# Kernel tuning notes

Measured on AMD Instinct MI355X. Metric: run time of the kernel, lower is better.

The kernel has to match this reference:

```python
import math
import jax, jax.numpy as jnp
import numpy as np

RM = 100.0      # r_max
RN = 1000       # r_dsc
LMAX = 2
MATCH_FRAC = 0.1
PARA1 = 1.0
RD = RM / RN    # radial step
NE = 4096       # batch of trial energies


def setup_inputs() -> dict:
    key = jax.random.key(0)
    # small negative energies (bound-state regime) to keep the exponential
    # Numerov growth over 900 steps within fp32 range
    init_energy = -(jax.random.uniform(key, (NE,), dtype=jnp.float32) * 0.01 + 0.005)
    return {"init_energy": init_energy}


def _disc_solve(sol0, factor, limit):
    # sol0: (5, n_e, L) initial 5-point window; factor: (rn, n_e, L)
    # Numerov-style 4-step recurrence, vectorized coefficients + lax.scan
    c = 3.0 / 40.0 * RD ** 2
    idx = jnp.arange(1, limit - 5)
    f0 = factor[idx]
    f1 = factor[idx + 1]
    f2 = factor[idx + 2]
    f3 = factor[idx + 3]
    f4 = factor[idx + 4]
    denom = 1.0 - c * f4
    a = -1.0 + c * f0 / denom
    b = 2.0 + (13.0 / 15.0) * RD ** 2 * f1 / denom
    cc = -2.0 + (7.0 / 60.0) * RD ** 2 * f2 / denom
    d = 2.0 + (13.0 / 15.0) * RD ** 2 * f3 / denom

    def step(prev, coef):
        ca, cb, ccc, cd = coef
        new4 = ca * prev[1] + cb * prev[2] + ccc * prev[3] + cd * prev[4]
        new = jnp.concatenate([prev[1:], new4[None]], axis=0)  # shift window
        return new, new

    _, rest = jax.lax.scan(step, sol0, (a, b, cc, d))
    return jnp.concatenate([sol0[None], rest], axis=0)  # (limit-5, 5, n_e, L)


def _derivative(func, at):
    return (25.0 * func[at - 1] - 48.0 * func[at - 2] + 36.0 * func[at - 3]
            - 16.0 * func[at - 4] + 3.0 * func[at - 5]) / (12.0 * RD)


def _integrate(func):
    # faithful to original: integrand squares `func` again (func is u**2 here)
    M = func.shape[0] // 4 - 1
    g0 = func[0:4 * M:4]
    g1 = func[1:4 * M:4]
    g2 = func[2:4 * M:4]
    g3 = func[3:4 * M:4]
    g4 = func[4::4][:M]
    integrand = (7.0 * (g0 ** 2 + g4 ** 2) + 32.0 * (g1 ** 2 + g3 ** 2)
                 + 12.0 * g2) * (2.0 * RD / 45.0)
    return integrand.sum(axis=0)


def _forward(init_energy):
    L = LMAX + 1
    dt = init_energy.dtype
    n_e = init_energy.shape[0]
    r = jnp.linspace(RM / RN, RM, RN, dtype=dt).reshape(RN, 1, 1)
    l = jnp.arange(L, dtype=dt).reshape(1, 1, L)

    energy = jnp.broadcast_to(init_energy[:, None], (n_e, L))  # (n_e, L)
    e_val = energy[None]                                       # (1, n_e, L)
    # coulomb potential -1/r; factor: (rn, n_e, L)
    factor = l * (l + 1) / r ** 2 + PARA1 * (-e_val - 1.0 / r)

    # left (r->0) initial window: u ~ r^(l+1) + r^(l+2)/(2(l+1)) * (-para_1)
    r0 = jnp.linspace(RD, 5 * RD, 5, dtype=dt).reshape(5, 1, 1)
    u_zero_init = jnp.broadcast_to(
        r0 ** (l + 1) - r0 ** (l + 2) / (2.0 * (l + 1)) * PARA1, (5, n_e, L))

    # right (r->r_max) initial window: r * truncated spherical-bessel series
    r_inf = jnp.linspace(RM - 4 * RD, RM, 5, dtype=dt).reshape(5, 1, 1)
    fact = jnp.array([math.prod([2 * li + 1 for li in range(lm + 1)])
                      for lm in range(L)], dtype=dt)  # [1, 3, 15]
    x = r_inf * jnp.sqrt(jnp.abs(e_val))              # (5, n_e, L)
    base = x ** l / fact
    t1 = x ** 2 / 2.0 / (2 * l + 3)
    t2 = (x ** 2 / 2.0) ** 2 / (2.0 * (2 * l + 3) * (2 * l + 5))
    u_infty_init = jnp.broadcast_to(r_inf * (base * (1.0 + t1 + t2)), (5, n_e, L))

    match = int(RN * MATCH_FRAC)  # 100
    uz = _disc_solve(u_zero_init, factor, match)                     # (95, 5, n_e, L)
    ui = _disc_solve(u_infty_init, factor[::-1], RN - match)[::-1]   # (895, 5, n_e, L)
    u_zero = jnp.concatenate([uz[0], uz[:, 4]], axis=0)    # (100, n_e, L)
    u_infty = jnp.concatenate([ui[0], ui[:, 4]], axis=0)   # (900, n_e, L)

    lfunc_in = _derivative(u_zero, match) / u_zero[-1]
    # faithful: the trailing flip acts on the energy axis of the (n_e, L) result
    lfunc_out = _derivative(u_infty[::-1], RN - match)[::-1] / u_infty[0]
    integ_in = _integrate(u_zero ** 2)
    integ_out = _integrate(u_infty ** 2)
    delta = -(lfunc_out - lfunc_in) / (integ_in / u_zero[-1] ** 2
                                       + integ_out / u_infty[0] ** 2)
    return (energy + delta, u_zero, u_infty)


def reference(init_energy):
    return _forward(init_energy)
```

## Files before the change

### kernel.cpp

```cpp
#include <hip/hip_runtime.h>


namespace {
constexpr int kNE    = 4096;
constexpr int kNCH   = kNE * 3;
constexpr int kMatch = 100;
constexpr float kC   = 3.0f / 40.0f * 0.01f;
constexpr float kK1  = 13.0f / 15.0f * 0.01f;
constexpr float kK2  = 7.0f / 60.0f * 0.01f;
constexpr int kSeg        = 32;
constexpr int kCPB        = 16;
constexpr int kZeroBlocks = kNCH / 512;
constexpr int kInfBlocks  = kNCH / kCPB;
}

__device__ __forceinline__ float rcp_f(float x) { return __builtin_amdgcn_rcpf(x); }
__device__ __forceinline__ float rcp_nr(float x) {
    float r = __builtin_amdgcn_rcpf(x);
    return fmaf(fmaf(-x, r, 1.0f), r, r);
}

__global__ __launch_bounds__(512, 4) void solve_kernel(const float* __restrict__ energy,
                                                       float* __restrict__ out,
                                                       float* __restrict__ ws)
{
    __shared__ __align__(16) float gtp[908];
    __shared__ float sM[kSeg][4][kCPB][4];
    float* sF = &sM[0][0][0][0];

    const int bid = (int)blockIdx.x;
    const int tid = (int)threadIdx.x;
    float* uzero = out + kNCH;
    float* uinf  = out + kNCH + (size_t)kMatch * kNCH;

    if (bid < kZeroBlocks) {
        const int t  = bid * 512 + tid;
        const int l  = t % 3;
        const int ei = t / 3;
        const float e = energy[ei], negE = -e;
        const float ll1 = (float)(l * (l + 1));
        const float rdiv = (l == 0) ? 0.5f : ((l == 1) ? 0.25f : (1.0f/6.0f));
        float p0,p1,p2,p3,p4;
        {
            float pw[5];
            #pragma unroll
            for (int k = 0; k < 5; ++k) {
                float r = 0.1f * (float)(k + 1);
                float rl1 = (l == 0) ? r : ((l == 1) ? r*r : r*r*r);
                pw[k] = rl1 - (rl1 * r) * rdiv;
                uzero[(size_t)k * kNCH + t] = pw[k];
            }
            uzero[(size_t)5 * kNCH + t] = pw[4];
            p0=pw[0]; p1=pw[1]; p2=pw[2]; p3=pw[3]; p4=pw[4];
        }
        float acc4, acc2;
        {
            float q0=p0*p0, q1=p1*p1, q2=p2*p2, q3=p3*p3, q4=p4*p4;
            acc4 = 7.0f*q0*q0 + 32.0f*q1*q1 + 32.0f*q3*q3 + 14.0f*q4*q4 + 32.0f*q4*q4;
            acc2 = q2;
        }
        float f0, f1, f2, f3;
        {
            float i1 = rcp_f(0.2f), i2 = rcp_f(0.3f), i3 = rcp_f(0.4f), i4 = rcp_f(0.5f);
            f0 = fmaf(i1, fmaf(ll1, i1, -1.0f), negE);
            f1 = fmaf(i2, fmaf(ll1, i2, -1.0f), negE);
            f2 = fmaf(i3, fmaf(ll1, i3, -1.0f), negE);
            f3 = fmaf(i4, fmaf(ll1, i4, -1.0f), negE);
        }
        float* ptr = uzero + (size_t)6 * kNCH + t;
        #pragma unroll 4
        for (int j = 5; j <= 98; ++j) {
            float ri = rcp_f(fmaf((float)j, 0.1f, 0.1f));
            float f4 = fmaf(ri, fmaf(ll1, ri, -1.0f), negE);
            float iv = rcp_f(fmaf(-kC, f4, 1.0f));
            float a  = fmaf(kC  * f0, iv, -1.0f);
            float b  = fmaf(kK1 * f1, iv,  2.0f);
            float cc = fmaf(kK2 * f2, iv, -2.0f);
            float d  = fmaf(kK1 * f3, iv,  2.0f);
            float nw = fmaf(d, p4, fmaf(cc, p3, fmaf(b, p2, a * p1)));
            *ptr = nw; ptr += kNCH;
            float v2 = nw*nw, v4 = v2*v2;
            if (j <= 94) {
                int m = (j + 1) & 3;
                if (m == 2)      acc2 += v2;
                else if (m == 0) acc4 += 14.0f * v4;
                else             acc4 += 32.0f * v4;
            } else if (j == 95) {
                acc4 += 7.0f * v4;
            }
            f0 = f1; f1 = f2; f2 = f3; f3 = f4;
            p0 = p1; p1 = p2; p2 = p3; p3 = p4; p4 = nw;
        }
        float integ = fmaf(12.0f, acc2, acc4) * (2.0f * 0.1f / 45.0f);
        float deriv = fmaf(25.0f, p4, fmaf(-48.0f, p3, fmaf(36.0f, p2,
                      fmaf(-16.0f, p1, 3.0f * p0)))) * (1.0f / 1.2f);
        ws[2 * kNCH + t] = deriv / p4;
        ws[3 * kNCH + t] = integ / (p4 * p4);
        return;
    }

    for (int k = tid; k < 908; k += 512) {
        int j = k - 3;
        gtp[k] = (j >= 1 && j <= 898) ? rcp_nr(fmaf((float)j, -0.1f, 100.0f)) : 1.0f;
    }
    __syncthreads();

    const int b = bid - kZeroBlocks;
    const int g = tid & (kCPB - 1);
    const int s = tid >> 4;
    const int t = b * kCPB + g;
    const int l  = t % 3;
    const int ei = t / 3;
    const float e = energy[ei], negE = -e;
    const float ll1 = (float)(l * (l + 1));
    const int jstart = 5 + 28 * s;

    const float4* gq = (const float4*)(&gtp[jstart + 3]);
    float ff0, ff1, ff2, ff3;
    {
        const float4 wF = *(const float4*)(&gtp[jstart - 1]);
        ff0 = fmaf(wF.x, fmaf(ll1, wF.x, -1.0f), negE);
        ff1 = fmaf(wF.y, fmaf(ll1, wF.y, -1.0f), negE);
        ff2 = fmaf(wF.z, fmaf(ll1, wF.z, -1.0f), negE);
        ff3 = fmaf(wF.w, fmaf(ll1, wF.w, -1.0f), negE);
    }
    float F0 = ff0, F1 = ff1, F2 = ff2, F3 = ff3;

    float ca, cb, cc_, cd;
#define COEF(RI, FA,FB,FC,FD) \
    { float f4 = fmaf(RI, fmaf(ll1, RI, -1.0f), negE); \
      float x  = kC * f4; \
      float iv = fmaf(x, x, x) + 1.0f; \
      ca  = fmaf(kC  * FA, iv, -1.0f); \
      cb  = fmaf(kK1 * FB, iv,  2.0f); \
      cc_ = fmaf(kK2 * FC, iv, -2.0f); \
      cd  = fmaf(kK1 * FD, iv,  2.0f); \
      FA = f4; }

#define MSTEP(RI, FA,FB,FC,FD, RA,RB,RC,RD) \
    { COEF(RI, FA,FB,FC,FD) \
      RA[0] = fmaf(cd,RD[0], fmaf(cc_,RC[0], fmaf(cb,RB[0], ca*RA[0]))); \
      RA[1] = fmaf(cd,RD[1], fmaf(cc_,RC[1], fmaf(cb,RB[1], ca*RA[1]))); \
      RA[2] = fmaf(cd,RD[2], fmaf(cc_,RC[2], fmaf(cb,RB[2], ca*RA[2]))); \
      RA[3] = fmaf(cd,RD[3], fmaf(cc_,RC[3], fmaf(cb,RB[3], ca*RA[3]))); }

    if (s != 31) {
        float ra[4] = {1,0,0,0}, rb[4] = {0,1,0,0}, rc[4] = {0,0,1,0}, rd[4] = {0,0,0,1};
        #pragma unroll
        for (int gi = 0; gi < 7; ++gi) {
            const float4 w = gq[gi];
            MSTEP(w.x, F0,F1,F2,F3, ra,rb,rc,rd)
            MSTEP(w.y, F1,F2,F3,F0, rb,rc,rd,ra)
            MSTEP(w.z, F2,F3,F0,F1, rc,rd,ra,rb)
            MSTEP(w.w, F3,F0,F1,F2, rd,ra,rb,rc)
        }
        *(float4*)&sM[s][0][g][0] = make_float4(ra[0], ra[1], ra[2], ra[3]);
        *(float4*)&sM[s][1][g][0] = make_float4(rb[0], rb[1], rb[2], rb[3]);
        *(float4*)&sM[s][2][g][0] = make_float4(rc[0], rc[1], rc[2], rc[3]);
        *(float4*)&sM[s][3][g][0] = make_float4(rd[0], rd[1], rd[2], rd[3]);
    }
    __syncthreads();

    if (s == 0) {
        const float se  = sqrtf(fabsf(e));
        const float rfc = (l == 0) ? 1.0f : ((l == 1) ? (1.0f/3.0f) : (1.0f/15.0f));
        const float rt1 = (l == 0) ? (1.0f/3.0f) : ((l == 1) ? (1.0f/5.0f) : (1.0f/7.0f));
        const float rt2 = (l == 0) ? (1.0f/30.0f) : ((l == 1) ? (1.0f/70.0f) : (1.0f/126.0f));
        float pw[5];
        #pragma unroll
        for (int k = 0; k < 5; ++k) {
            float rinf = 99.6f + 0.1f * (float)k;
            float x  = rinf * se;
            float xl = (l == 0) ? 1.0f : ((l == 1) ? x : x * x);
            float h  = x * x * 0.5f;
            pw[k] = rinf * (xl * rfc * (1.0f + h * rt1 + (h * h) * rt2));
        }
        uinf[(size_t)899 * kNCH + t] = pw[4];
        float st0 = pw[1], st1 = pw[2], st2 = pw[3], st3 = pw[4];
        for (int ss = 0; ss < kSeg; ++ss) {
            if (ss < kSeg - 1) {
                float4 M0 = *(const float4*)&sM[ss][0][g][0];
                float4 M1 = *(const float4*)&sM[ss][1][g][0];
                float4 M2 = *(const float4*)&sM[ss][2][g][0];
                float4 M3 = *(const float4*)&sM[ss][3][g][0];
                *(float4*)&sM[ss][0][g][0] = make_float4(st0, st1, st2, st3);
                float n0 = fmaf(M0.w,st3, fmaf(M0.z,st2, fmaf(M0.y,st1, M0.x*st0)));
                float n1 = fmaf(M1.w,st3, fmaf(M1.z,st2, fmaf(M1.y,st1, M1.x*st0)));
                float n2 = fmaf(M2.w,st3, fmaf(M2.z,st2, fmaf(M2.y,st1, M2.x*st0)));
                float n3 = fmaf(M3.w,st3, fmaf(M3.z,st2, fmaf(M3.y,st1, M3.x*st0)));
                st0 = n0; st1 = n1; st2 = n2; st3 = n3;
            } else {
                *(float4*)&sM[ss][0][g][0] = make_float4(st0, st1, st2, st3);
            }
        }
    }
    __syncthreads();

    float W0[4] = {0.0f, 32.0f, 14.0f, 32.0f};
    float V0[4] = {1.0f, 0.0f, 0.0f, 0.0f};
    float WR[4] = {0.0f, 32.0f, 14.0f, 32.0f};
    float VR[4] = {1.0f, 0.0f, 0.0f, 0.0f};
    if (s == 0) {
        W0[0]=0.0f; V0[0]=0.0f; W0[1]=0.0f; W0[2]=7.0f; W0[3]=32.0f;
    }

    F0 = ff0; F1 = ff1; F2 = ff2; F3 = ff3;
    float p0, p1, p2, p3;
    {
        float4 P = *(const float4*)&sM[s][0][g][0];
        p0 = P.x; p1 = P.y; p2 = P.z; p3 = P.w;
    }
    float acc4 = 0.0f, acc2 = 0.0f;
    float* ptr = uinf + (size_t)(903 - jstart) * kNCH + t;
#define RSTEPW(RI, FA,FB,FC,FD, PA,PB,PC,PD, W,V,K) \
    { COEF(RI, FA,FB,FC,FD) \
      float nw = fmaf(cd,PD, fmaf(cc_,PC, fmaf(cb,PB, ca*PA))); \
      PA = nw; *ptr = nw; ptr -= kNCH; \
      float v2 = nw*nw, v4 = v2*v2; \
      acc4 = fmaf(W[K], v4, acc4); \
      acc2 = fmaf(V[K], v2, acc2); }
#define PG(G, W, V) \
    { const float4 w = gq[G]; \
      RSTEPW(w.x, F0,F1,F2,F3, p0,p1,p2,p3, W,V,0) \
      RSTEPW(w.y, F1,F2,F3,F0, p1,p2,p3,p0, W,V,1) \
      RSTEPW(w.z, F2,F3,F0,F1, p2,p3,p0,p1, W,V,2) \
      RSTEPW(w.w, F3,F0,F1,F2, p3,p0,p1,p2, W,V,3) }

    PG(0, W0, V0)
    PG(1, WR, VR) PG(2, WR, VR) PG(3, WR, VR) PG(4, WR, VR) PG(5, WR, VR)
    float h0 = p1, h1 = p2, h2 = p3;
    if (s == 31) { WR[2] = 0.0f; WR[3] = 0.0f; }
    PG(6, WR, VR)
    float h3 = p0, h4 = p1;
#undef PG
#undef RSTEPW

    {
        float2 rr; rr.x = acc4; rr.y = acc2;
        *(float2*)&sF[s * 256 + 64 + 4 * g] = rr;
    }
    __syncthreads();

    if (s == kSeg - 1) {
        float a4 = 0.0f, a2 = 0.0f;
        #pragma unroll
        for (int ss = 0; ss < kSeg; ++ss) {
            float2 rr = *(const float2*)&sF[ss * 256 + 64 + 4 * g];
            a4 += rr.x; a2 += rr.y;
        }
        uinf[(size_t)0 * kNCH + t] = h0;
        uinf[(size_t)1 * kNCH + t] = h1;
        uinf[(size_t)2 * kNCH + t] = h2;
        uinf[(size_t)3 * kNCH + t] = h3;
        uinf[(size_t)4 * kNCH + t] = h4;
        float q0 = h0*h0, q1 = h1*h1, q2 = h2*h2, q3 = h3*h3, q4 = h4*h4;
        a4 += 7.0f*q0*q0 + 32.0f*q1*q1 + 32.0f*q3*q3 + 14.0f*q4*q4;
        a2 += q2;
        float integ = fmaf(12.0f, a2, a4) * (2.0f * 0.1f / 45.0f);
        float deriv = fmaf(25.0f, h0, fmaf(-48.0f, h1, fmaf(36.0f, h2,
                      fmaf(-16.0f, h3, 3.0f * h4)))) * (1.0f / 1.2f);
        ws[t]        = deriv / h0;
        ws[kNCH + t] = integ / (h0 * h0);
    }
#undef MSTEP
#undef COEF
}

__global__ __launch_bounds__(256) void final_kernel(const float* __restrict__ energy,
                                                    const float* __restrict__ ws,
                                                    float* __restrict__ out)
{
    int t = (int)blockIdx.x * 256 + (int)threadIdx.x;
    if (t >= kNCH) return;
    int l = t % 3, ei = t / 3;
    float lf_out = ws[(kNE - 1 - ei) * 3 + l];
    float lf_in  = ws[2 * kNCH + t];
    float den    = ws[kNCH + t] + ws[3 * kNCH + t];
    out[t] = energy[ei] - (lf_out - lf_in) / den;
}

extern "C" void kernel_launch(void* const* d_in, const int* in_sizes, int n_in,
                              void* d_out, int out_size, void* d_ws, size_t ws_size,
                              hipStream_t stream) {
    (void)in_sizes; (void)n_in; (void)out_size; (void)ws_size;
    const float* energy = (const float*)d_in[0];
    float* out = (float*)d_out;
    float* ws  = (float*)d_ws;
    solve_kernel<<<kZeroBlocks + kInfBlocks, 512, 0, stream>>>(energy, out, ws);
    final_kernel<<<kNCH / 256, 256, 0, stream>>>(energy, ws, out);
}
```

Measured before the change: 85.82 us.

## Process two channels per thread in the u_infty segmented solve

Each thread in the outward (u_infty) blocks now handles two adjacent channels instead of one, which halves the number of inf blocks. The per-step recurrence and the transfer-matrix products for the two channels are interleaved to expose more ILP, and u_infty stores become float2 writes so global memory traffic is wider. This costs roughly double the register use and extra shared memory per block, which may lower occupancy.

```diff
diff --git a/kernel.cpp b/kernel.cpp
--- a/kernel.cpp
+++ b/kernel.cpp
@@ -9,9 +9,9 @@
 constexpr float kK1  = 13.0f / 15.0f * 0.01f;
 constexpr float kK2  = 7.0f / 60.0f * 0.01f;
 constexpr int kSeg        = 32;
-constexpr int kCPB        = 16;
+constexpr int kPPB        = 16;
 constexpr int kZeroBlocks = kNCH / 512;
-constexpr int kInfBlocks  = kNCH / kCPB;
+constexpr int kInfBlocks  = kNCH / (2 * kPPB);
 }
 
 __device__ __forceinline__ float rcp_f(float x) { return __builtin_amdgcn_rcpf(x); }
@@ -25,8 +25,9 @@
                                                        float* __restrict__ ws)
 {
     __shared__ __align__(16) float gtp[908];
-    __shared__ float sM[kSeg][4][kCPB][4];
-    float* sF = &sM[0][0][0][0];
+    __shared__ float sMA[kSeg][4][kPPB][4];
+    __shared__ float sMB[kSeg][4][kPPB][4];
+    __shared__ float4 sRed[kSeg][kPPB];
 
     const int bid = (int)blockIdx.x;
     const int tid = (int)threadIdx.x;
@@ -105,92 +106,130 @@
     }
     __syncthreads();
 
-    const int b = bid - kZeroBlocks;
-    const int g = tid & (kCPB - 1);
-    const int s = tid >> 4;
-    const int t = b * kCPB + g;
-    const int l  = t % 3;
-    const int ei = t / 3;
-    const float e = energy[ei], negE = -e;
-    const float ll1 = (float)(l * (l + 1));
+    const int b  = bid - kZeroBlocks;
+    const int g  = tid & (kPPB - 1);
+    const int s  = tid >> 4;
+    const int t2 = b * (2 * kPPB) + g * 2;
+    const int lA = t2 % 3,  lB = (t2 + 1) % 3;
+    const float eA = energy[t2 / 3], eB = energy[(t2 + 1) / 3];
+    const float negEA = -eA, negEB = -eB;
+    const float ll1A = (float)(lA * (lA + 1));
+    const float ll1B = (float)(lB * (lB + 1));
     const int jstart = 5 + 28 * s;
 
     const float4* gq = (const float4*)(&gtp[jstart + 3]);
-    float ff0, ff1, ff2, ff3;
+    float fA0, fA1, fA2, fA3, fB0, fB1, fB2, fB3;
     {
         const float4 wF = *(const float4*)(&gtp[jstart - 1]);
-        ff0 = fmaf(wF.x, fmaf(ll1, wF.x, -1.0f), negE);
-        ff1 = fmaf(wF.y, fmaf(ll1, wF.y, -1.0f), negE);
-        ff2 = fmaf(wF.z, fmaf(ll1, wF.z, -1.0f), negE);
-        ff3 = fmaf(wF.w, fmaf(ll1, wF.w, -1.0f), negE);
-    }
-    float F0 = ff0, F1 = ff1, F2 = ff2, F3 = ff3;
-
-    float ca, cb, cc_, cd;
-#define COEF(RI, FA,FB,FC,FD) \
-    { float f4 = fmaf(RI, fmaf(ll1, RI, -1.0f), negE); \
-      float x  = kC * f4; \
-      float iv = fmaf(x, x, x) + 1.0f; \
-      ca  = fmaf(kC  * FA, iv, -1.0f); \
-      cb  = fmaf(kK1 * FB, iv,  2.0f); \
-      cc_ = fmaf(kK2 * FC, iv, -2.0f); \
-      cd  = fmaf(kK1 * FD, iv,  2.0f); \
-      FA = f4; }
-
-#define MSTEP(RI, FA,FB,FC,FD, RA,RB,RC,RD) \
-    { COEF(RI, FA,FB,FC,FD) \
-      RA[0] = fmaf(cd,RD[0], fmaf(cc_,RC[0], fmaf(cb,RB[0], ca*RA[0]))); \
-      RA[1] = fmaf(cd,RD[1], fmaf(cc_,RC[1], fmaf(cb,RB[1], ca*RA[1]))); \
-      RA[2] = fmaf(cd,RD[2], fmaf(cc_,RC[2], fmaf(cb,RB[2], ca*RA[2]))); \
-      RA[3] = fmaf(cd,RD[3], fmaf(cc_,RC[3], fmaf(cb,RB[3], ca*RA[3]))); }
+        fA0 = fmaf(wF.x, fmaf(ll1A, wF.x, -1.0f), negEA);
+        fA1 = fmaf(wF.y, fmaf(ll1A, wF.y, -1.0f), negEA);
+        fA2 = fmaf(wF.z, fmaf(ll1A, wF.z, -1.0f), negEA);
+        fA3 = fmaf(wF.w, fmaf(ll1A, wF.w, -1.0f), negEA);
+        fB0 = fmaf(wF.x, fmaf(ll1B, wF.x, -1.0f), negEB);
+        fB1 = fmaf(wF.y, fmaf(ll1B, wF.y, -1.0f), negEB);
+        fB2 = fmaf(wF.z, fmaf(ll1B, wF.z, -1.0f), negEB);
+        fB3 = fmaf(wF.w, fmaf(ll1B, wF.w, -1.0f), negEB);
+    }
+    float FA0 = fA0, FA1 = fA1, FA2 = fA2, FA3 = fA3;
+    float FB0 = fB0, FB1 = fB1, FB2 = fB2, FB3 = fB3;
+
+    float caA, cbA, ccA, cdA, caB, cbB, ccB, cdB;
+#define COEF2(RI, A0,A1,A2,A3, B0,B1,B2,B3) \
+    { float f4A = fmaf(RI, fmaf(ll1A, RI, -1.0f), negEA); \
+      float f4B = fmaf(RI, fmaf(ll1B, RI, -1.0f), negEB); \
+      float xA = kC * f4A, xB = kC * f4B; \
+      float ivA = fmaf(xA, xA, xA) + 1.0f; \
+      float ivB = fmaf(xB, xB, xB) + 1.0f; \
+      caA = fmaf(kC  * A0, ivA, -1.0f);  caB = fmaf(kC  * B0, ivB, -1.0f); \
+      cbA = fmaf(kK1 * A1, ivA,  2.0f);  cbB = fmaf(kK1 * B1, ivB,  2.0f); \
+      ccA = fmaf(kK2 * A2, ivA, -2.0f);  ccB = fmaf(kK2 * B2, ivB, -2.0f); \
+      cdA = fmaf(kK1 * A3, ivA,  2.0f);  cdB = fmaf(kK1 * B3, ivB,  2.0f); \
+      A0 = f4A; B0 = f4B; }
+
+#define MSTEP2(RI, A0,A1,A2,A3, B0,B1,B2,B3, RA,RB,RC,RD, QA,QB,QC,QD) \
+    { COEF2(RI, A0,A1,A2,A3, B0,B1,B2,B3) \
+      RA[0] = fmaf(cdA,RD[0], fmaf(ccA,RC[0], fmaf(cbA,RB[0], caA*RA[0]))); \
+      QA[0] = fmaf(cdB,QD[0], fmaf(ccB,QC[0], fmaf(cbB,QB[0], caB*QA[0]))); \
+      RA[1] = fmaf(cdA,RD[1], fmaf(ccA,RC[1], fmaf(cbA,RB[1], caA*RA[1]))); \
+      QA[1] = fmaf(cdB,QD[1], fmaf(ccB,QC[1], fmaf(cbB,QB[1], caB*QA[1]))); \
+      RA[2] = fmaf(cdA,RD[2], fmaf(ccA,RC[2], fmaf(cbA,RB[2], caA*RA[2]))); \
+      QA[2] = fmaf(cdB,QD[2], fmaf(ccB,QC[2], fmaf(cbB,QB[2], caB*QA[2]))); \
+      RA[3] = fmaf(cdA,RD[3], fmaf(ccA,RC[3], fmaf(cbA,RB[3], caA*RA[3]))); \
+      QA[3] = fmaf(cdB,QD[3], fmaf(ccB,QC[3], fmaf(cbB,QB[3], caB*QA[3]))); }
 
     if (s != 31) {
-        float ra[4] = {1,0,0,0}, rb[4] = {0,1,0,0}, rc[4] = {0,0,1,0}, rd[4] = {0,0,0,1};
+        float raA[4]={1,0,0,0}, rbA[4]={0,1,0,0}, rcA[4]={0,0,1,0}, rdA[4]={0,0,0,1};
+        float raB[4]={1,0,0,0}, rbB[4]={0,1,0,0}, rcB[4]={0,0,1,0}, rdB[4]={0,0,0,1};
         #pragma unroll
         for (int gi = 0; gi < 7; ++gi) {
             const float4 w = gq[gi];
-            MSTEP(w.x, F0,F1,F2,F3, ra,rb,rc,rd)
-            MSTEP(w.y, F1,F2,F3,F0, rb,rc,rd,ra)
-            MSTEP(w.z, F2,F3,F0,F1, rc,rd,ra,rb)
-            MSTEP(w.w, F3,F0,F1,F2, rd,ra,rb,rc)
-        }
-        *(float4*)&sM[s][0][g][0] = make_float4(ra[0], ra[1], ra[2], ra[3]);
-        *(float4*)&sM[s][1][g][0] = make_float4(rb[0], rb[1], rb[2], rb[3]);
-        *(float4*)&sM[s][2][g][0] = make_float4(rc[0], rc[1], rc[2], rc[3]);
-        *(float4*)&sM[s][3][g][0] = make_float4(rd[0], rd[1], rd[2], rd[3]);
-    }
+            MSTEP2(w.x, FA0,FA1,FA2,FA3, FB0,FB1,FB2,FB3, raA,rbA,rcA,rdA, raB,rbB,rcB,rdB)
+            MSTEP2(w.y, FA1,FA2,FA3,FA0, FB1,FB2,FB3,FB0, rbA,rcA,rdA,raA, rbB,rcB,rdB,raB)
+            MSTEP2(w.z, FA2,FA3,FA0,FA1, FB2,FB3,FB0,FB1, rcA,rdA,raA,rbA, rcB,rdB,raB,rbB)
+            MSTEP2(w.w, FA3,FA0,FA1,FA2, FB3,FB0,FB1,FB2, rdA,raA,rbA,rcA, rdB,raB,rbB,rcB)
+        }
+        *(float4*)&sMA[s][0][g][0] = make_float4(raA[0], raA[1], raA[2], raA[3]);
+        *(float4*)&sMA[s][1][g][0] = make_float4(rbA[0], rbA[1], rbA[2], rbA[3]);
+        *(float4*)&sMA[s][2][g][0] = make_float4(rcA[0], rcA[1], rcA[2], rcA[3]);
+        *(float4*)&sMA[s][3][g][0] = make_float4(rdA[0], rdA[1], rdA[2], rdA[3]);
+        *(float4*)&sMB[s][0][g][0] = make_float4(raB[0], raB[1], raB[2], raB[3]);
+        *(float4*)&sMB[s][1][g][0] = make_float4(rbB[0], rbB[1], rbB[2], rbB[3]);
+        *(float4*)&sMB[s][2][g][0] = make_float4(rcB[0], rcB[1], rcB[2], rcB[3]);
+        *(float4*)&sMB[s][3][g][0] = make_float4(rdB[0], rdB[1], rdB[2], rdB[3]);
+    }
+#undef MSTEP2
     __syncthreads();
 
     if (s == 0) {
-        const float se  = sqrtf(fabsf(e));
-        const float rfc = (l == 0) ? 1.0f : ((l == 1) ? (1.0f/3.0f) : (1.0f/15.0f));
-        const float rt1 = (l == 0) ? (1.0f/3.0f) : ((l == 1) ? (1.0f/5.0f) : (1.0f/7.0f));
-        const float rt2 = (l == 0) ? (1.0f/30.0f) : ((l == 1) ? (1.0f/70.0f) : (1.0f/126.0f));
-        float pw[5];
-        #pragma unroll
-        for (int k = 0; k < 5; ++k) {
-            float rinf = 99.6f + 0.1f * (float)k;
-            float x  = rinf * se;
-            float xl = (l == 0) ? 1.0f : ((l == 1) ? x : x * x);
-            float h  = x * x * 0.5f;
-            pw[k] = rinf * (xl * rfc * (1.0f + h * rt1 + (h * h) * rt2));
-        }
-        uinf[(size_t)899 * kNCH + t] = pw[4];
-        float st0 = pw[1], st1 = pw[2], st2 = pw[3], st3 = pw[4];
+        float stA0, stA1, stA2, stA3, stB0, stB1, stB2, stB3;
+        {
+            const float seA = sqrtf(fabsf(eA)), seB = sqrtf(fabsf(eB));
+            const float rfcA = (lA == 0) ? 1.0f : ((lA == 1) ? (1.0f/3.0f) : (1.0f/15.0f));
+            const float rt1A = (lA == 0) ? (1.0f/3.0f) : ((lA == 1) ? (1.0f/5.0f) : (1.0f/7.0f));
+            const float rt2A = (lA == 0) ? (1.0f/30.0f) : ((lA == 1) ? (1.0f/70.0f) : (1.0f/126.0f));
+            const float rfcB = (lB == 0) ? 1.0f : ((lB == 1) ? (1.0f/3.0f) : (1.0f/15.0f));
+            const float rt1B = (lB == 0) ? (1.0f/3.0f) : ((lB == 1) ? (1.0f/5.0f) : (1.0f/7.0f));
+            const float rt2B = (lB == 0) ? (1.0f/30.0f) : ((lB == 1) ? (1.0f/70.0f) : (1.0f/126.0f));
+            float pwA[5], pwB[5];
+            #pragma unroll
+            for (int k = 0; k < 5; ++k) {
+                float rinf = 99.6f + 0.1f * (float)k;
+                float xA = rinf * seA, xB = rinf * seB;
+                float xlA = (lA == 0) ? 1.0f : ((lA == 1) ? xA : xA * xA);
+                float xlB = (lB == 0) ? 1.0f : ((lB == 1) ? xB : xB * xB);
+                float hA = xA * xA * 0.5f, hB = xB * xB * 0.5f;
+                pwA[k] = rinf * (xlA * rfcA * (1.0f + hA * rt1A + (hA * hA) * rt2A));
+                pwB[k] = rinf * (xlB * rfcB * (1.0f + hB * rt1B + (hB * hB) * rt2B));
+            }
+            *(float2*)&uinf[(size_t)899 * kNCH + t2] = make_float2(pwA[4], pwB[4]);
+            stA0 = pwA[1]; stA1 = pwA[2]; stA2 = pwA[3]; stA3 = pwA[4];
+            stB0 = pwB[1]; stB1 = pwB[2]; stB2 = pwB[3]; stB3 = pwB[4];
+        }
         for (int ss = 0; ss < kSeg; ++ss) {
             if (ss < kSeg - 1) {
-                float4 M0 = *(const float4*)&sM[ss][0][g][0];
-                float4 M1 = *(const float4*)&sM[ss][1][g][0];
-                float4 M2 = *(const float4*)&sM[ss][2][g][0];
-                float4 M3 = *(const float4*)&sM[ss][3][g][0];
-                *(float4*)&sM[ss][0][g][0] = make_float4(st0, st1, st2, st3);
-                float n0 = fmaf(M0.w,st3, fmaf(M0.z,st2, fmaf(M0.y,st1, M0.x*st0)));
-                float n1 = fmaf(M1.w,st3, fmaf(M1.z,st2, fmaf(M1.y,st1, M1.x*st0)));
-                float n2 = fmaf(M2.w,st3, fmaf(M2.z,st2, fmaf(M2.y,st1, M2.x*st0)));
-                float n3 = fmaf(M3.w,st3, fmaf(M3.z,st2, fmaf(M3.y,st1, M3.x*st0)));
-                st0 = n0; st1 = n1; st2 = n2; st3 = n3;
+                float4 MA0 = *(const float4*)&sMA[ss][0][g][0];
+                float4 MA1 = *(const float4*)&sMA[ss][1][g][0];
+                float4 MA2 = *(const float4*)&sMA[ss][2][g][0];
+                float4 MA3 = *(const float4*)&sMA[ss][3][g][0];
+                float4 MB0 = *(const float4*)&sMB[ss][0][g][0];
+                float4 MB1 = *(const float4*)&sMB[ss][1][g][0];
+                float4 MB2 = *(const float4*)&sMB[ss][2][g][0];
+                float4 MB3 = *(const float4*)&sMB[ss][3][g][0];
+                *(float4*)&sMA[ss][0][g][0] = make_float4(stA0, stA1, stA2, stA3);
+                *(float4*)&sMB[ss][0][g][0] = make_float4(stB0, stB1, stB2, stB3);
+                float nA0 = fmaf(MA0.w,stA3, fmaf(MA0.z,stA2, fmaf(MA0.y,stA1, MA0.x*stA0)));
+                float nA1 = fmaf(MA1.w,stA3, fmaf(MA1.z,stA2, fmaf(MA1.y,stA1, MA1.x*stA0)));
+                float nA2 = fmaf(MA2.w,stA3, fmaf(MA2.z,stA2, fmaf(MA2.y,stA1, MA2.x*stA0)));
+                float nA3 = fmaf(MA3.w,stA3, fmaf(MA3.z,stA2, fmaf(MA3.y,stA1, MA3.x*stA0)));
+                float nB0 = fmaf(MB0.w,stB3, fmaf(MB0.z,stB2, fmaf(MB0.y,stB1, MB0.x*stB0)));
+                float nB1 = fmaf(MB1.w,stB3, fmaf(MB1.z,stB2, fmaf(MB1.y,stB1, MB1.x*stB0)));
+                float nB2 = fmaf(MB2.w,stB3, fmaf(MB2.z,stB2, fmaf(MB2.y,stB1, MB2.x*stB0)));
+                float nB3 = fmaf(MB3.w,stB3, fmaf(MB3.z,stB2, fmaf(MB3.y,stB1, MB3.x*stB0)));
+                stA0 = nA0; stA1 = nA1; stA2 = nA2; stA3 = nA3;
+                stB0 = nB0; stB1 = nB1; stB2 = nB2; stB3 = nB3;
             } else {
-                *(float4*)&sM[ss][0][g][0] = make_float4(st0, st1, st2, st3);
+                *(float4*)&sMA[ss][0][g][0] = make_float4(stA0, stA1, stA2, stA3);
+                *(float4*)&sMB[ss][0][g][0] = make_float4(stB0, stB1, stB2, stB3);
             }
         }
     }
@@ -204,66 +243,76 @@
         W0[0]=0.0f; V0[0]=0.0f; W0[1]=0.0f; W0[2]=7.0f; W0[3]=32.0f;
     }
 
-    F0 = ff0; F1 = ff1; F2 = ff2; F3 = ff3;
-    float p0, p1, p2, p3;
+    FA0 = fA0; FA1 = fA1; FA2 = fA2; FA3 = fA3;
+    FB0 = fB0; FB1 = fB1; FB2 = fB2; FB3 = fB3;
+    float pA0, pA1, pA2, pA3, pB0, pB1, pB2, pB3;
     {
-        float4 P = *(const float4*)&sM[s][0][g][0];
-        p0 = P.x; p1 = P.y; p2 = P.z; p3 = P.w;
-    }
-    float acc4 = 0.0f, acc2 = 0.0f;
-    float* ptr = uinf + (size_t)(903 - jstart) * kNCH + t;
-#define RSTEPW(RI, FA,FB,FC,FD, PA,PB,PC,PD, W,V,K) \
-    { COEF(RI, FA,FB,FC,FD) \
-      float nw = fmaf(cd,PD, fmaf(cc_,PC, fmaf(cb,PB, ca*PA))); \
-      PA = nw; *ptr = nw; ptr -= kNCH; \
-      float v2 = nw*nw, v4 = v2*v2; \
-      acc4 = fmaf(W[K], v4, acc4); \
-      acc2 = fmaf(V[K], v2, acc2); }
+        float4 PA = *(const float4*)&sMA[s][0][g][0];
+        float4 PB = *(const float4*)&sMB[s][0][g][0];
+        pA0 = PA.x; pA1 = PA.y; pA2 = PA.z; pA3 = PA.w;
+        pB0 = PB.x; pB1 = PB.y; pB2 = PB.z; pB3 = PB.w;
+    }
+    float acc4A = 0.0f, acc2A = 0.0f, acc4B = 0.0f, acc2B = 0.0f;
+    float* ptr = uinf + (size_t)(903 - jstart) * kNCH + t2;
+#define RSTEP2(RI, A0,A1,A2,A3, B0,B1,B2,B3, PA,PB,PC,PD, QA,QB,QC,QD, W,V,K) \
+    { COEF2(RI, A0,A1,A2,A3, B0,B1,B2,B3) \
+      float nwA = fmaf(cdA,PD, fmaf(ccA,PC, fmaf(cbA,PB, caA*PA))); \
+      float nwB = fmaf(cdB,QD, fmaf(ccB,QC, fmaf(cbB,QB, caB*QA))); \
+      PA = nwA; QA = nwB; \
+      *(float2*)ptr = make_float2(nwA, nwB); ptr -= kNCH; \
+      float v2A = nwA*nwA, v4A = v2A*v2A; \
+      float v2B = nwB*nwB, v4B = v2B*v2B; \
+      acc4A = fmaf(W[K], v4A, acc4A);  acc4B = fmaf(W[K], v4B, acc4B); \
+      acc2A = fmaf(V[K], v2A, acc2A);  acc2B = fmaf(V[K], v2B, acc2B); }
 #define PG(G, W, V) \
     { const float4 w = gq[G]; \
-      RSTEPW(w.x, F0,F1,F2,F3, p0,p1,p2,p3, W,V,0) \
-      RSTEPW(w.y, F1,F2,F3,F0, p1,p2,p3,p0, W,V,1) \
-      RSTEPW(w.z, F2,F3,F0,F1, p2,p3,p0,p1, W,V,2) \
-      RSTEPW(w.w, F3,F0,F1,F2, p3,p0,p1,p2, W,V,3) }
+      RSTEP2(w.x, FA0,FA1,FA2,FA3, FB0,FB1,FB2,FB3, pA0,pA1,pA2,pA3, pB0,pB1,pB2,pB3, W,V,0) \
+      RSTEP2(w.y, FA1,FA2,FA3,FA0, FB1,FB2,FB3,FB0, pA1,pA2,pA3,pA0, pB1,pB2,pB3,pB0, W,V,1) \
+      RSTEP2(w.z, FA2,FA3,FA0,FA1, FB2,FB3,FB0,FB1, pA2,pA3,pA0,pA1, pB2,pB3,pB0,pB1, W,V,2) \
+      RSTEP2(w.w, FA3,FA0,FA1,FA2, FB3,FB0,FB1,FB2, pA3,pA0,pA1,pA2, pB3,pB0,pB1,pB2, W,V,3) }
 
     PG(0, W0, V0)
     PG(1, WR, VR) PG(2, WR, VR) PG(3, WR, VR) PG(4, WR, VR) PG(5, WR, VR)
-    float h0 = p1, h1 = p2, h2 = p3;
+    float hA0 = pA1, hA1 = pA2, hA2 = pA3;
+    float hB0 = pB1, hB1 = pB2, hB2 = pB3;
     if (s == 31) { WR[2] = 0.0f; WR[3] = 0.0f; }
     PG(6, WR, VR)
-    float h3 = p0, h4 = p1;
+    float hA3 = pA0, hA4 = pA1, hB3 = pB0, hB4 = pB1;
 #undef PG
-#undef RSTEPW
-
-    {
-        float2 rr; rr.x = acc4; rr.y = acc2;
-        *(float2*)&sF[s * 256 + 64 + 4 * g] = rr;
-    }
+#undef RSTEP2
+#undef COEF2
+
+    sRed[s][g] = make_float4(acc4A, acc2A, acc4B, acc2B);
     __syncthreads();
 
     if (s == kSeg - 1) {
-        float a4 = 0.0f, a2 = 0.0f;
+        float a4A = 0.0f, a2A = 0.0f, a4B = 0.0f, a2B = 0.0f;
         #pragma unroll
         for (int ss = 0; ss < kSeg; ++ss) {
-            float2 rr = *(const float2*)&sF[ss * 256 + 64 + 4 * g];
-            a4 += rr.x; a2 += rr.y;
-        }
-        uinf[(size_t)0 * kNCH + t] = h0;
-        uinf[(size_t)1 * kNCH + t] = h1;
-        uinf[(size_t)2 * kNCH + t] = h2;
-        uinf[(size_t)3 * kNCH + t] = h3;
-        uinf[(size_t)4 * kNCH + t] = h4;
-        float q0 = h0*h0, q1 = h1*h1, q2 = h2*h2, q3 = h3*h3, q4 = h4*h4;
-        a4 += 7.0f*q0*q0 + 32.0f*q1*q1 + 32.0f*q3*q3 + 14.0f*q4*q4;
-        a2 += q2;
-        float integ = fmaf(12.0f, a2, a4) * (2.0f * 0.1f / 45.0f);
-        float deriv = fmaf(25.0f, h0, fmaf(-48.0f, h1, fmaf(36.0f, h2,
-                      fmaf(-16.0f, h3, 3.0f * h4)))) * (1.0f / 1.2f);
-        ws[t]        = deriv / h0;
-        ws[kNCH + t] = integ / (h0 * h0);
-    }
-#undef MSTEP
-#undef COEF
+            float4 rr = sRed[ss][g];
+            a4A += rr.x; a2A += rr.y; a4B += rr.z; a2B += rr.w;
+        }
+        *(float2*)&uinf[(size_t)0 * kNCH + t2] = make_float2(hA0, hB0);
+        *(float2*)&uinf[(size_t)1 * kNCH + t2] = make_float2(hA1, hB1);
+        *(float2*)&uinf[(size_t)2 * kNCH + t2] = make_float2(hA2, hB2);
+        *(float2*)&uinf[(size_t)3 * kNCH + t2] = make_float2(hA3, hB3);
+        *(float2*)&uinf[(size_t)4 * kNCH + t2] = make_float2(hA4, hB4);
+        float qA0=hA0*hA0, qA1=hA1*hA1, qA2=hA2*hA2, qA3=hA3*hA3, qA4=hA4*hA4;
+        float qB0=hB0*hB0, qB1=hB1*hB1, qB2=hB2*hB2, qB3=hB3*hB3, qB4=hB4*hB4;
+        a4A += 7.0f*qA0*qA0 + 32.0f*qA1*qA1 + 32.0f*qA3*qA3 + 14.0f*qA4*qA4;
+        a4B += 7.0f*qB0*qB0 + 32.0f*qB1*qB1 + 32.0f*qB3*qB3 + 14.0f*qB4*qB4;
+        a2A += qA2; a2B += qB2;
+        float integA = fmaf(12.0f, a2A, a4A) * (2.0f * 0.1f / 45.0f);
+        float integB = fmaf(12.0f, a2B, a4B) * (2.0f * 0.1f / 45.0f);
+        float derivA = fmaf(25.0f, hA0, fmaf(-48.0f, hA1, fmaf(36.0f, hA2,
+                       fmaf(-16.0f, hA3, 3.0f * hA4)))) * (1.0f / 1.2f);
+        float derivB = fmaf(25.0f, hB0, fmaf(-48.0f, hB1, fmaf(36.0f, hB2,
+                       fmaf(-16.0f, hB3, 3.0f * hB4)))) * (1.0f / 1.2f);
+        ws[t2]            = derivA / hA0;
+        ws[t2 + 1]        = derivB / hB0;
+        ws[kNCH + t2]     = integA / (hA0 * hA0);
+        ws[kNCH + t2 + 1] = integB / (hB0 * hB0);
+    }
 }
 
 __global__ __launch_bounds__(256) void final_kernel(const float* __restrict__ energy,
```

New measurement: 88.96 us. +3.7%, slower.
